# Kernel tuning notes

Measured on AMD Instinct MI355X. Metric: run time of the kernel, lower is better.

## Reference

```python
import jax, jax.numpy as jnp
import numpy as np

NHEAD = 16
HEAD_DIM = 64
EMBED_DIM = NHEAD * HEAD_DIM  # 1024
U, R, L, M = 2048, 256, 1024, 512


def setup_inputs() -> dict:
    key = jax.random.key(0)
    ks = jax.random.split(key, 11)
    D = EMBED_DIM
    inp = {
        "utterance": jax.random.normal(ks[0], (U, 1, D), jnp.float32),
        "right_context": jax.random.normal(ks[1], (R, 1, D), jnp.float32),
        "memory": jax.random.normal(ks[2], (M, 1, D), jnp.float32),
        "left_context_key": jax.random.normal(ks[3], (L, 1, D), jnp.float32),
        "left_context_val": jax.random.normal(ks[4], (L, 1, D), jnp.float32),
        "Wq": jax.random.normal(ks[5], (D, D), jnp.float32) * 0.02,
        "bq": jax.random.normal(ks[6], (D,), jnp.float32) * 0.02,
        "Wkv": jax.random.normal(ks[7], (2 * D, D), jnp.float32) * 0.02,
        "bkv": jax.random.normal(ks[8], (2 * D,), jnp.float32) * 0.02,
        "Wo": jax.random.normal(ks[9], (D, D), jnp.float32) * 0.02,
        "bo": jax.random.normal(ks[10], (D,), jnp.float32) * 0.02,
    }
    return inp


def reference(utterance, right_context, memory, left_context_key, left_context_val,
              Wq, bq, Wkv, bkv, Wo, bo):
    D = EMBED_DIM
    scaling = HEAD_DIM ** (-0.5)

    # query = Linear([right_context; utterance])  -> (Q, 1, D), Q = R + U
    q_in = jnp.concatenate([right_context, utterance], axis=0)
    query = q_in @ Wq.T + bq

    # key/value = Linear([memory; right_context; utterance]) split in two
    kv_in = jnp.concatenate([memory, right_context, utterance], axis=0)
    kv = kv_in @ Wkv.T + bkv  # (M+R+U, 1, 2D)
    k_new, v_new = kv[..., :D], kv[..., D:]

    # insert cached left-context key/value after [memory; right_context]
    key = jnp.concatenate([k_new[: M + R], left_context_key, k_new[M + R:]], axis=0)
    value = jnp.concatenate([v_new[: M + R], left_context_val, v_new[M + R:]], axis=0)

    Q = U + R
    KV = M + R + L + U
    # (T, 1, D) -> (nhead, T, head_dim)
    q = query.reshape(Q, NHEAD, HEAD_DIM).transpose(1, 0, 2)
    k = key.reshape(KV, NHEAD, HEAD_DIM).transpose(1, 0, 2)
    v = value.reshape(KV, NHEAD, HEAD_DIM).transpose(1, 0, 2)

    weights = jnp.einsum("hqd,hkd->hqk", q * scaling, k)  # (nhead, Q, KV)
    probs = jax.nn.softmax(weights, axis=-1)
    attn = jnp.einsum("hqk,hkd->hqd", probs, v)  # (nhead, Q, head_dim)

    attn = attn.transpose(1, 0, 2).reshape(Q, D)[:, None, :]  # (Q, 1, D)
    out = attn @ Wo.T + bo
    return out, key, value
```

## Files before the change

### kernel.cpp

```cpp
#include <hip/hip_runtime.h>
#include <hip/hip_bf16.h>

#define EMBED   1024
#define NHEADS  16
#define HDIM    64
#define U_LEN   2048
#define R_LEN   256
#define L_LEN   1024
#define M_LEN   512
#define Q_LEN   (U_LEN + R_LEN)
#define KV_LEN  (M_LEN + R_LEN + L_LEN + U_LEN)
#define X_ROWS  (M_LEN + R_LEN + U_LEN)
#define NPART   6
#define KV_PART (KV_LEN / NPART)

typedef __attribute__((ext_vector_type(8))) short short8;
typedef __attribute__((ext_vector_type(4))) float f32x4;
typedef __attribute__((ext_vector_type(16))) float f32x16;

#define QSCALE 0.180336880f

__device__ __forceinline__ void gl2lds16(const __hip_bfloat16* g, __hip_bfloat16* l) {
  __builtin_amdgcn_global_load_lds(
      (const __attribute__((address_space(1))) unsigned int*)g,
      (__attribute__((address_space(3))) unsigned int*)l, 16, 0, 0);
}

__device__ __forceinline__ unsigned pack_bf16(float a, float b) {
  unsigned r;
  asm("v_cvt_pk_bf16_f32 %0, %1, %2" : "=v"(r) : "v"(a), "v"(b));
  return r;
}

__device__ __forceinline__ void plane_swap(unsigned a, unsigned b, int h2,
                                           unsigned& lo, unsigned& hi) {
#if __has_builtin(__builtin_amdgcn_permlane32_swap)
  auto r = __builtin_amdgcn_permlane32_swap(a, b, false, false);
  lo = r[0]; hi = r[1];
#else
  unsigned s0 = h2 ? a : b;
  unsigned r0 = __shfl_xor(s0, 32, 64);
  lo = h2 ? r0 : a;
  hi = h2 ? b : r0;
#endif
}

__global__ __launch_bounds__(256) void prep_kernel(
    const float* __restrict__ mem, const float* __restrict__ rc,
    const float* __restrict__ utt, const float* __restrict__ lk,
    const float* __restrict__ lv, const float* __restrict__ Wq,
    const float* __restrict__ Wkv, const float* __restrict__ Wo,
    __hip_bfloat16* __restrict__ X, __hip_bfloat16* __restrict__ WB,
    __hip_bfloat16* __restrict__ WoB,
    float* __restrict__ key_out, float* __restrict__ val_out,
    __hip_bfloat16* __restrict__ k_bf, __hip_bfloat16* __restrict__ v_bf) {
  int b = blockIdx.x, tid = threadIdx.x;
  if (b < 2816) {
    int row = b, col = tid * 4;
    const float* src;
    if (row < M_LEN)              src = mem + row * EMBED;
    else if (row < M_LEN + R_LEN) src = rc + (row - M_LEN) * EMBED;
    else                          src = utt + (row - M_LEN - R_LEN) * EMBED;
    float4 v = *reinterpret_cast<const float4*>(src + col);
    __hip_bfloat16* d = X + (size_t)row * EMBED + col;
    d[0] = __float2bfloat16(v.x); d[1] = __float2bfloat16(v.y);
    d[2] = __float2bfloat16(v.z); d[3] = __float2bfloat16(v.w);
  } else if (b < 6912) {
    const float* src; __hip_bfloat16* dst;
    int blk;
    if (b < 3840)      { src = Wq;  dst = WB;                blk = b - 2816; }
    else if (b < 5888) { src = Wkv; dst = WB + 1024 * 1024;  blk = b - 3840; }
    else               { src = Wo;  dst = WoB;               blk = b - 5888; }
    int idx = blk * 1024 + tid * 4;
    float4 v = *reinterpret_cast<const float4*>(src + idx);
    dst[idx + 0] = __float2bfloat16(v.x);
    dst[idx + 1] = __float2bfloat16(v.y);
    dst[idx + 2] = __float2bfloat16(v.z);
    dst[idx + 3] = __float2bfloat16(v.w);
  } else {
    int row = b - 6912, c0 = tid * 4;
    int orow = 768 + row;
    float4 kv4 = *reinterpret_cast<const float4*>(lk + row * EMBED + c0);
    float4 vv4 = *reinterpret_cast<const float4*>(lv + row * EMBED + c0);
    *reinterpret_cast<float4*>(key_out + (size_t)orow * EMBED + c0) = kv4;
    *reinterpret_cast<float4*>(val_out + (size_t)orow * EMBED + c0) = vv4;
    __hip_bfloat16* kd = k_bf + (size_t)orow * EMBED + c0;
    __hip_bfloat16* vd = v_bf + (size_t)orow * EMBED + c0;
    kd[0] = __float2bfloat16(kv4.x); kd[1] = __float2bfloat16(kv4.y);
    kd[2] = __float2bfloat16(kv4.z); kd[3] = __float2bfloat16(kv4.w);
    vd[0] = __float2bfloat16(vv4.x); vd[1] = __float2bfloat16(vv4.y);
    vd[2] = __float2bfloat16(vv4.z); vd[3] = __float2bfloat16(vv4.w);
  }
}

__global__ __launch_bounds__(256) void transpose_kernel(
    const unsigned short* __restrict__ v_bf, unsigned short* __restrict__ vT) {
  __shared__ unsigned short T[64][72];
  int kt = blockIdx.x * 64, d0 = blockIdx.y * 64;
  int t = threadIdx.x;
  int r = t >> 3, c = (t & 7) * 8;
#pragma unroll
  for (int half = 0; half < 2; half++) {
    int kv = r + half * 32;
    short8 v = *reinterpret_cast<const short8*>(v_bf + (size_t)(kt + kv) * EMBED + d0 + c);
#pragma unroll
    for (int j = 0; j < 8; j++) T[c + j][kv] = (unsigned short)v[j];
  }
  __syncthreads();
#pragma unroll
  for (int half = 0; half < 2; half++) {
    int d = r + half * 32;
    *reinterpret_cast<short8*>(vT + (size_t)(d0 + d) * KV_LEN + kt + c) =
        *reinterpret_cast<const short8*>(&T[d][c]);
  }
}

__global__ __launch_bounds__(256) void gemm_qkv(
    const __hip_bfloat16* __restrict__ A, const __hip_bfloat16* __restrict__ B,
    const float* __restrict__ bq, const float* __restrict__ bkv,
    float* __restrict__ key_out, float* __restrict__ val_out,
    __hip_bfloat16* __restrict__ q_bf, __hip_bfloat16* __restrict__ k_bf,
    __hip_bfloat16* __restrict__ v_bf) {
  __shared__ __align__(16) __hip_bfloat16 As[128 * 64];
  __shared__ __align__(16) __hip_bfloat16 Bs[64 * 64];
  const int K = EMBED;
  int tid = threadIdx.x;
  int wave = tid >> 6, lane = tid & 63, quad = lane >> 4, l16 = lane & 15;
  int wm = wave >> 1, wn = wave & 1;
  int mbase = blockIdx.y * 128, nbase = blockIdx.x * 64;

  if (nbase < 1024 && mbase + 128 <= 512) return;

  int srow = tid >> 3;
  int scol = ((tid & 7) ^ (srow & 7)) * 8;
  const __hip_bfloat16* aG = A + (size_t)(mbase + srow) * K + scol;
  const __hip_bfloat16* bG = B + (size_t)(nbase + srow) * K + scol;
  int swz = l16 & 7;

  f32x4 acc[4][2] = {};
  for (int kt = 0; kt < K; kt += 64) {
    gl2lds16(aG + kt, As + tid * 8);
    gl2lds16(aG + (size_t)32 * K + kt, As + (tid + 256) * 8);
    gl2lds16(aG + (size_t)64 * K + kt, As + (tid + 512) * 8);
    gl2lds16(aG + (size_t)96 * K + kt, As + (tid + 768) * 8);
    gl2lds16(bG + kt, Bs + tid * 8);
    gl2lds16(bG + (size_t)32 * K + kt, Bs + (tid + 256) * 8);
    __syncthreads();
#pragma unroll
    for (int ks = 0; ks < 2; ks++) {
      short8 af[4], bfr[2];
#pragma unroll
      for (int i = 0; i < 4; i++)
        af[i] = *reinterpret_cast<const short8*>(
            As + (wm * 64 + i * 16 + l16) * 64 + ((ks * 4 + quad) ^ swz) * 8);
#pragma unroll
      for (int j = 0; j < 2; j++)
        bfr[j] = *reinterpret_cast<const short8*>(
            Bs + (wn * 32 + j * 16 + l16) * 64 + ((ks * 4 + quad) ^ swz) * 8);
#pragma unroll
      for (int i = 0; i < 4; i++)
#pragma unroll
        for (int j = 0; j < 2; j++)
          acc[i][j] = __builtin_amdgcn_mfma_f32_16x16x32_bf16(af[i], bfr[j], acc[i][j], 0, 0, 0);
    }
    __syncthreads();
  }

#pragma unroll
  for (int i = 0; i < 4; i++) {
    int rb = mbase + wm * 64 + i * 16 + quad * 4;
#pragma unroll
    for (int j = 0; j < 2; j++) {
      int cg = nbase + wn * 32 + j * 16 + l16;
      float bv = (cg < 1024) ? bq[cg] : bkv[cg - 1024];
#pragma unroll
      for (int reg = 0; reg < 4; reg++) {
        int rg = rb + reg;
        float val = acc[i][j][reg] + bv;
        if (cg < 1024) {
          if (rg >= 512)
            q_bf[(size_t)(rg - 512) * 1024 + cg] = __float2bfloat16(val * QSCALE);
        } else {
          int orow = (rg < 768) ? rg : rg + 1024;
          if (cg < 2048) {
            int cc = cg - 1024;
            key_out[(size_t)orow * 1024 + cc] = val;
            k_bf[(size_t)orow * 1024 + cc] = __float2bfloat16(val);
          } else {
            int cc = cg - 2048;
            val_out[(size_t)orow * 1024 + cc] = val;
            v_bf[(size_t)orow * 1024 + cc] = __float2bfloat16(val);
          }
        }
      }
    }
  }
}

__global__ __launch_bounds__(256) void gemm_out(
    const __hip_bfloat16* __restrict__ A, const __hip_bfloat16* __restrict__ B,
    float* __restrict__ partial) {
  __shared__ __align__(16) __hip_bfloat16 As[64 * 64];
  __shared__ __align__(16) __hip_bfloat16 Bs[64 * 64];
  const int K = EMBED, N = EMBED;
  int tid = threadIdx.x;
  int wave = tid >> 6, lane = tid & 63, quad = lane >> 4, l16 = lane & 15;
  int wm = wave >> 1, wn = wave & 1;
  int mbase = blockIdx.y * 64, nbase = blockIdx.x * 64;
  int kbase = blockIdx.z * 512;
  float* outp = partial + (size_t)blockIdx.z * Q_LEN * EMBED;

  int srow = tid >> 3;
  int scol = ((tid & 7) ^ (srow & 7)) * 8;
  const __hip_bfloat16* aG = A + (size_t)(mbase + srow) * K + kbase + scol;
  const __hip_bfloat16* bG = B + (size_t)(nbase + srow) * K + kbase + scol;
  int swz = l16 & 7;

  f32x4 acc[2][2] = {};
  for (int kt = 0; kt < 512; kt += 64) {
    gl2lds16(aG + kt, As + tid * 8);
    gl2lds16(aG + (size_t)32 * K + kt, As + (tid + 256) * 8);
    gl2lds16(bG + kt, Bs + tid * 8);
    gl2lds16(bG + (size_t)32 * K + kt, Bs + (tid + 256) * 8);
    __syncthreads();
#pragma unroll
    for (int ks = 0; ks < 2; ks++) {
      short8 af[2], bfr[2];
#pragma unroll
      for (int i = 0; i < 2; i++)
        af[i] = *reinterpret_cast<const short8*>(
            As + (wm * 32 + i * 16 + l16) * 64 + ((ks * 4 + quad) ^ swz) * 8);
#pragma unroll
      for (int j = 0; j < 2; j++)
        bfr[j] = *reinterpret_cast<const short8*>(
            Bs + (wn * 32 + j * 16 + l16) * 64 + ((ks * 4 + quad) ^ swz) * 8);
#pragma unroll
      for (int i = 0; i < 2; i++)
#pragma unroll
        for (int j = 0; j < 2; j++)
          acc[i][j] = __builtin_amdgcn_mfma_f32_16x16x32_bf16(af[i], bfr[j], acc[i][j], 0, 0, 0);
    }
    __syncthreads();
  }

#pragma unroll
  for (int i = 0; i < 2; i++) {
    int rb = mbase + wm * 32 + i * 16 + quad * 4;
#pragma unroll
    for (int j = 0; j < 2; j++) {
      int cg = nbase + wn * 32 + j * 16 + l16;
#pragma unroll
      for (int reg = 0; reg < 4; reg++)
        outp[(size_t)(rb + reg) * N + cg] = acc[i][j][reg];
    }
  }
}

__global__ __launch_bounds__(256) void reduce_out_kernel(
    const float* __restrict__ partial, const float* __restrict__ bias,
    float* __restrict__ outf) {
  int row = blockIdx.x, c = threadIdx.x * 4;
  float4 p0 = *reinterpret_cast<const float4*>(partial + (size_t)row * EMBED + c);
  float4 p1 = *reinterpret_cast<const float4*>(partial + (size_t)(Q_LEN + row) * EMBED + c);
  float4 bv = *reinterpret_cast<const float4*>(bias + c);
  float4 o;
  o.x = p0.x + p1.x + bv.x; o.y = p0.y + p1.y + bv.y;
  o.z = p0.z + p1.z + bv.z; o.w = p0.w + p1.w + bv.w;
  *reinterpret_cast<float4*>(outf + (size_t)row * EMBED + c) = o;
}

__global__ __launch_bounds__(256, 4) void attn_kernel(
    const __hip_bfloat16* __restrict__ q_bf, const __hip_bfloat16* __restrict__ k_bf,
    const __hip_bfloat16* __restrict__ vT,
    __hip_bfloat16* __restrict__ o_part, float* __restrict__ lsum) {
  __shared__ __align__(16) __hip_bfloat16 Ks[64][72];
  __shared__ __align__(16) __hip_bfloat16 VTs[64][72];
  int tid = threadIdx.x;
  int w = tid >> 6, lane = tid & 63, l31 = lane & 31, h2 = lane >> 5;

  int lid = blockIdx.x;
  int xcd = lid & 7, sfl = lid >> 3;
  int gi = sfl / 18, j = sfl - gi * 18;
  int g = gi * 8 + xcd;
  int part = g >> 4, h = g & 15;
  int qbase = j * 128;
  int qg = qbase + w * 32 + l31;

  short8 Qf[4];
#pragma unroll
  for (int ks = 0; ks < 4; ks++)
    Qf[ks] = *reinterpret_cast<const short8*>(
        q_bf + (size_t)qg * EMBED + h * HDIM + ks * 16 + h2 * 8);

  f32x16 ot[2] = {};
  float l_run = 0.f;

  int sr = tid >> 3, sc = (tid & 7) * 8;
  const int kv0 = part * KV_PART;

  short8 kr[2], vr[2];
#pragma unroll
  for (int half = 0; half < 2; half++) {
    int r = sr + half * 32;
    kr[half] = *reinterpret_cast<const short8*>(
        k_bf + (size_t)(kv0 + r) * EMBED + h * HDIM + sc);
    vr[half] = *reinterpret_cast<const short8*>(
        vT + (size_t)(h * HDIM + r) * KV_LEN + kv0 + sc);
  }

  for (int kt = kv0; kt < kv0 + KV_PART; kt += 64) {
    __syncthreads();
#pragma unroll
    for (int half = 0; half < 2; half++) {
      int r = sr + half * 32;
      *reinterpret_cast<short8*>(&Ks[r][sc]) = kr[half];
      *reinterpret_cast<short8*>(&VTs[r][sc]) = vr[half];
    }
    __syncthreads();
    if (kt + 64 < kv0 + KV_PART) {
#pragma unroll
      for (int half = 0; half < 2; half++) {
        int r = sr + half * 32;
        kr[half] = *reinterpret_cast<const short8*>(
            k_bf + (size_t)(kt + 64 + r) * EMBED + h * HDIM + sc);
        vr[half] = *reinterpret_cast<const short8*>(
            vT + (size_t)(h * HDIM + r) * KV_LEN + kt + 64 + sc);
      }
    }

#pragma unroll
    for (int kvs = 0; kvs < 2; kvs++) {
      f32x16 s = {};
      __builtin_amdgcn_s_setprio(1);
#pragma unroll
      for (int ks = 0; ks < 4; ks++) {
        short8 ak = *reinterpret_cast<const short8*>(&Ks[kvs * 32 + l31][ks * 16 + h2 * 8]);
        s = __builtin_amdgcn_mfma_f32_32x32x16_bf16(ak, Qf[ks], s, 0, 0, 0);
      }
      __builtin_amdgcn_s_setprio(0);
      unsigned u[4][2];
#pragma unroll
      for (int gq = 0; gq < 4; gq++) {
        float p0 = __builtin_amdgcn_exp2f(s[4 * gq + 0]);
        float p1 = __builtin_amdgcn_exp2f(s[4 * gq + 1]);
        float p2 = __builtin_amdgcn_exp2f(s[4 * gq + 2]);
        float p3 = __builtin_amdgcn_exp2f(s[4 * gq + 3]);
        l_run += (p0 + p1) + (p2 + p3);
        u[gq][0] = pack_bf16(p0, p1);
        u[gq][1] = pack_bf16(p2, p3);
      }
#pragma unroll
      for (int half = 0; half < 2; half++) {
        int c = kvs * 2 + half;
        int gA = 2 * half, gB = 2 * half + 1;
        uint4 fr;
        plane_swap(u[gA][0], u[gB][0], h2, fr.x, fr.z);
        plane_swap(u[gA][1], u[gB][1], h2, fr.y, fr.w);
        short8 pf = __builtin_bit_cast(short8, fr);
        __builtin_amdgcn_s_setprio(1);
#pragma unroll
        for (int ds = 0; ds < 2; ds++) {
          short8 av = *reinterpret_cast<const short8*>(&VTs[ds * 32 + l31][c * 16 + h2 * 8]);
          ot[ds] = __builtin_amdgcn_mfma_f32_32x32x16_bf16(av, pf, ot[ds], 0, 0, 0);
        }
        __builtin_amdgcn_s_setprio(0);
      }
    }
  }

  l_run += __shfl_xor(l_run, 32, 64);
  float inv = 1.0f / l_run;

  size_t orow = (size_t)part * Q_LEN + qg;
#pragma unroll
  for (int ds = 0; ds < 2; ds++)
#pragma unroll
    for (int gq = 0; gq < 4; gq++) {
      uint2 pk;
      pk.x = pack_bf16(ot[ds][4 * gq + 0] * inv, ot[ds][4 * gq + 1] * inv);
      pk.y = pack_bf16(ot[ds][4 * gq + 2] * inv, ot[ds][4 * gq + 3] * inv);
      *reinterpret_cast<uint2*>(
          o_part + orow * 1024 + h * HDIM + ds * 32 + gq * 8 + h2 * 4) = pk;
    }
  if (lane < 32)
    lsum[orow * NHEADS + h] = l_run;
}

__global__ __launch_bounds__(256) void merge_kernel(
    const __hip_bfloat16* __restrict__ o_part, const float* __restrict__ lsum,
    __hip_bfloat16* __restrict__ attn_bf) {
  int q = blockIdx.x;
  int c = threadIdx.x * 4;
  int h = c >> 6;
  float wt[NPART], L = 0.f;
#pragma unroll
  for (int p = 0; p < NPART; p++) {
    wt[p] = lsum[((size_t)p * Q_LEN + q) * NHEADS + h];
    L += wt[p];
  }
  float invL = 1.0f / L;
  float acc[4] = {0.f, 0.f, 0.f, 0.f};
#pragma unroll
  for (int p = 0; p < NPART; p++) {
    __hip_bfloat16 v[4];
    *reinterpret_cast<uint2*>(v) =
        *reinterpret_cast<const uint2*>(o_part + ((size_t)p * Q_LEN + q) * 1024 + c);
#pragma unroll
    for (int jj = 0; jj < 4; jj++) acc[jj] += wt[p] * __bfloat162float(v[jj]);
  }
  uint2 pk;
  pk.x = pack_bf16(acc[0] * invL, acc[1] * invL);
  pk.y = pack_bf16(acc[2] * invL, acc[3] * invL);
  *reinterpret_cast<uint2*>(attn_bf + (size_t)q * 1024 + c) = pk;
}


extern "C" void kernel_launch(void* const* d_in, const int* in_sizes, int n_in,
                              void* d_out, int out_size, void* d_ws, size_t ws_size,
                              hipStream_t stream) {
  const float* utt = (const float*)d_in[0];
  const float* rc  = (const float*)d_in[1];
  const float* mem = (const float*)d_in[2];
  const float* lk  = (const float*)d_in[3];
  const float* lv  = (const float*)d_in[4];
  const float* Wq  = (const float*)d_in[5];
  const float* bq  = (const float*)d_in[6];
  const float* Wkv = (const float*)d_in[7];
  const float* bkv = (const float*)d_in[8];
  const float* Wo  = (const float*)d_in[9];
  const float* bo  = (const float*)d_in[10];

  float* out_f   = (float*)d_out;
  float* key_out = out_f + Q_LEN * EMBED;
  float* val_out = key_out + KV_LEN * EMBED;

  char* ws = (char*)d_ws;
  size_t off = 0;
  __hip_bfloat16* X_bf   = (__hip_bfloat16*)(ws + off); off += (size_t)X_ROWS * EMBED * 2;
  __hip_bfloat16* WB_bf  = (__hip_bfloat16*)(ws + off); off += (size_t)3 * EMBED * EMBED * 2;
  __hip_bfloat16* Wo_bf  = (__hip_bfloat16*)(ws + off); off += (size_t)EMBED * EMBED * 2;
  __hip_bfloat16* q_bf   = (__hip_bfloat16*)(ws + off); off += (size_t)Q_LEN * EMBED * 2;
  __hip_bfloat16* k_bf   = (__hip_bfloat16*)(ws + off); off += (size_t)KV_LEN * EMBED * 2;
  __hip_bfloat16* vT_bf  = (__hip_bfloat16*)(ws + off); off += (size_t)EMBED * KV_LEN * 2;
  __hip_bfloat16* o_part = (__hip_bfloat16*)(ws + off); off += (size_t)NPART * Q_LEN * EMBED * 2;
  __hip_bfloat16* attn_bf = X_bf;
  float* lsum = (float*)WB_bf;
  __hip_bfloat16* v_bf = o_part;
  float* out_partial = (float*)q_bf;
  (void)off; (void)ws_size; (void)in_sizes; (void)n_in; (void)out_size;

  prep_kernel<<<7936, 256, 0, stream>>>(mem, rc, utt, lk, lv, Wq, Wkv, Wo,
                                        X_bf, WB_bf, Wo_bf,
                                        key_out, val_out, k_bf, v_bf);
  gemm_qkv<<<dim3(3 * EMBED / 64, X_ROWS / 128), 256, 0, stream>>>(
      X_bf, WB_bf, bq, bkv, key_out, val_out, q_bf, k_bf, v_bf);
  transpose_kernel<<<dim3(KV_LEN / 64, EMBED / 64), 256, 0, stream>>>(
      (const unsigned short*)v_bf, (unsigned short*)vT_bf);
  attn_kernel<<<dim3((Q_LEN / 128) * NHEADS * NPART), 256, 0, stream>>>(
      q_bf, k_bf, vT_bf, o_part, lsum);
  merge_kernel<<<Q_LEN, 256, 0, stream>>>(o_part, lsum, attn_bf);
  gemm_out<<<dim3(EMBED / 64, Q_LEN / 64, 2), 256, 0, stream>>>(
      attn_bf, Wo_bf, out_partial);
  reduce_out_kernel<<<Q_LEN, 256, 0, stream>>>(out_partial, bo, out_f);
}
```

Before: 212.3 us.

## Enlarge QKV GEMM tiles, drop split-K in out-proj, pack bf16 stores, swizzle grids

The QKV projection GEMM moves from 128x64 to 128x128 tiles, so each wave computes a 4x4 MFMA block and reuses more of its LDS data. Both GEMMs now use a 1D grid remapped so consecutive blocks land on the same XCD. The output projection no longer splits K in two: it runs the full K loop, adds the bias itself, and the separate reduce kernel is removed. The prep kernel writes packed bf16 pairs as 8-byte stores instead of scalar 2-byte stores. The risks are fewer blocks in flight (528 and 576) with more registers per thread, and longer per-block K loops in the output GEMM.

```diff
diff --git a/kernel.cpp b/kernel.cpp
--- a/kernel.cpp
+++ b/kernel.cpp
@@ -62,9 +62,8 @@
     else if (row < M_LEN + R_LEN) src = rc + (row - M_LEN) * EMBED;
     else                          src = utt + (row - M_LEN - R_LEN) * EMBED;
     float4 v = *reinterpret_cast<const float4*>(src + col);
-    __hip_bfloat16* d = X + (size_t)row * EMBED + col;
-    d[0] = __float2bfloat16(v.x); d[1] = __float2bfloat16(v.y);
-    d[2] = __float2bfloat16(v.z); d[3] = __float2bfloat16(v.w);
+    uint2 pk; pk.x = pack_bf16(v.x, v.y); pk.y = pack_bf16(v.z, v.w);
+    *reinterpret_cast<uint2*>(X + (size_t)row * EMBED + col) = pk;
   } else if (b < 6912) {
     const float* src; __hip_bfloat16* dst;
     int blk;
@@ -73,10 +72,8 @@
     else               { src = Wo;  dst = WoB;               blk = b - 5888; }
     int idx = blk * 1024 + tid * 4;
     float4 v = *reinterpret_cast<const float4*>(src + idx);
-    dst[idx + 0] = __float2bfloat16(v.x);
-    dst[idx + 1] = __float2bfloat16(v.y);
-    dst[idx + 2] = __float2bfloat16(v.z);
-    dst[idx + 3] = __float2bfloat16(v.w);
+    uint2 pk; pk.x = pack_bf16(v.x, v.y); pk.y = pack_bf16(v.z, v.w);
+    *reinterpret_cast<uint2*>(dst + idx) = pk;
   } else {
     int row = b - 6912, c0 = tid * 4;
     int orow = 768 + row;
@@ -84,12 +81,11 @@
     float4 vv4 = *reinterpret_cast<const float4*>(lv + row * EMBED + c0);
     *reinterpret_cast<float4*>(key_out + (size_t)orow * EMBED + c0) = kv4;
     *reinterpret_cast<float4*>(val_out + (size_t)orow * EMBED + c0) = vv4;
-    __hip_bfloat16* kd = k_bf + (size_t)orow * EMBED + c0;
-    __hip_bfloat16* vd = v_bf + (size_t)orow * EMBED + c0;
-    kd[0] = __float2bfloat16(kv4.x); kd[1] = __float2bfloat16(kv4.y);
-    kd[2] = __float2bfloat16(kv4.z); kd[3] = __float2bfloat16(kv4.w);
-    vd[0] = __float2bfloat16(vv4.x); vd[1] = __float2bfloat16(vv4.y);
-    vd[2] = __float2bfloat16(vv4.z); vd[3] = __float2bfloat16(vv4.w);
+    uint2 pk, pv;
+    pk.x = pack_bf16(kv4.x, kv4.y); pk.y = pack_bf16(kv4.z, kv4.w);
+    pv.x = pack_bf16(vv4.x, vv4.y); pv.y = pack_bf16(vv4.z, vv4.w);
+    *reinterpret_cast<uint2*>(k_bf + (size_t)orow * EMBED + c0) = pk;
+    *reinterpret_cast<uint2*>(v_bf + (size_t)orow * EMBED + c0) = pv;
   }
 }
 
@@ -122,14 +118,18 @@
     __hip_bfloat16* __restrict__ q_bf, __hip_bfloat16* __restrict__ k_bf,
     __hip_bfloat16* __restrict__ v_bf) {
   __shared__ __align__(16) __hip_bfloat16 As[128 * 64];
-  __shared__ __align__(16) __hip_bfloat16 Bs[64 * 64];
+  __shared__ __align__(16) __hip_bfloat16 Bs[128 * 64];
   const int K = EMBED;
   int tid = threadIdx.x;
   int wave = tid >> 6, lane = tid & 63, quad = lane >> 4, l16 = lane & 15;
   int wm = wave >> 1, wn = wave & 1;
-  int mbase = blockIdx.y * 128, nbase = blockIdx.x * 64;
-
-  if (nbase < 1024 && mbase + 128 <= 512) return;
+
+  int lid = blockIdx.x;
+  int gsw = (lid & 7) * 66 + (lid >> 3);
+  int bx = gsw / 22, by = gsw % 22;
+  int mbase = by * 128, nbase = bx * 128;
+
+  if (nbase + 128 <= 1024 && mbase + 128 <= 512) return;
 
   int srow = tid >> 3;
   int scol = ((tid & 7) ^ (srow & 7)) * 8;
@@ -137,30 +137,29 @@
   const __hip_bfloat16* bG = B + (size_t)(nbase + srow) * K + scol;
   int swz = l16 & 7;
 
-  f32x4 acc[4][2] = {};
+  f32x4 acc[4][4] = {};
   for (int kt = 0; kt < K; kt += 64) {
-    gl2lds16(aG + kt, As + tid * 8);
-    gl2lds16(aG + (size_t)32 * K + kt, As + (tid + 256) * 8);
-    gl2lds16(aG + (size_t)64 * K + kt, As + (tid + 512) * 8);
-    gl2lds16(aG + (size_t)96 * K + kt, As + (tid + 768) * 8);
-    gl2lds16(bG + kt, Bs + tid * 8);
-    gl2lds16(bG + (size_t)32 * K + kt, Bs + (tid + 256) * 8);
+#pragma unroll
+    for (int i = 0; i < 4; i++) {
+      gl2lds16(aG + (size_t)(32 * i) * K + kt, As + (tid + 256 * i) * 8);
+      gl2lds16(bG + (size_t)(32 * i) * K + kt, Bs + (tid + 256 * i) * 8);
+    }
     __syncthreads();
 #pragma unroll
     for (int ks = 0; ks < 2; ks++) {
-      short8 af[4], bfr[2];
+      short8 af[4], bfr[4];
 #pragma unroll
       for (int i = 0; i < 4; i++)
         af[i] = *reinterpret_cast<const short8*>(
             As + (wm * 64 + i * 16 + l16) * 64 + ((ks * 4 + quad) ^ swz) * 8);
 #pragma unroll
-      for (int j = 0; j < 2; j++)
+      for (int j = 0; j < 4; j++)
         bfr[j] = *reinterpret_cast<const short8*>(
-            Bs + (wn * 32 + j * 16 + l16) * 64 + ((ks * 4 + quad) ^ swz) * 8);
+            Bs + (wn * 64 + j * 16 + l16) * 64 + ((ks * 4 + quad) ^ swz) * 8);
 #pragma unroll
       for (int i = 0; i < 4; i++)
 #pragma unroll
-        for (int j = 0; j < 2; j++)
+        for (int j = 0; j < 4; j++)
           acc[i][j] = __builtin_amdgcn_mfma_f32_16x16x32_bf16(af[i], bfr[j], acc[i][j], 0, 0, 0);
     }
     __syncthreads();
@@ -170,8 +169,8 @@
   for (int i = 0; i < 4; i++) {
     int rb = mbase + wm * 64 + i * 16 + quad * 4;
 #pragma unroll
-    for (int j = 0; j < 2; j++) {
-      int cg = nbase + wn * 32 + j * 16 + l16;
+    for (int j = 0; j < 4; j++) {
+      int cg = nbase + wn * 64 + j * 16 + l16;
       float bv = (cg < 1024) ? bq[cg] : bkv[cg - 1024];
 #pragma unroll
       for (int reg = 0; reg < 4; reg++) {
@@ -199,25 +198,27 @@
 
 __global__ __launch_bounds__(256) void gemm_out(
     const __hip_bfloat16* __restrict__ A, const __hip_bfloat16* __restrict__ B,
-    float* __restrict__ partial) {
+    const float* __restrict__ bias, float* __restrict__ outf) {
   __shared__ __align__(16) __hip_bfloat16 As[64 * 64];
   __shared__ __align__(16) __hip_bfloat16 Bs[64 * 64];
   const int K = EMBED, N = EMBED;
   int tid = threadIdx.x;
   int wave = tid >> 6, lane = tid & 63, quad = lane >> 4, l16 = lane & 15;
   int wm = wave >> 1, wn = wave & 1;
-  int mbase = blockIdx.y * 64, nbase = blockIdx.x * 64;
-  int kbase = blockIdx.z * 512;
-  float* outp = partial + (size_t)blockIdx.z * Q_LEN * EMBED;
+
+  int lid = blockIdx.x;
+  int gsw = (lid & 7) * 72 + (lid >> 3);
+  int bx = gsw / 36, by = gsw % 36;
+  int mbase = by * 64, nbase = bx * 64;
 
   int srow = tid >> 3;
   int scol = ((tid & 7) ^ (srow & 7)) * 8;
-  const __hip_bfloat16* aG = A + (size_t)(mbase + srow) * K + kbase + scol;
-  const __hip_bfloat16* bG = B + (size_t)(nbase + srow) * K + kbase + scol;
+  const __hip_bfloat16* aG = A + (size_t)(mbase + srow) * K + scol;
+  const __hip_bfloat16* bG = B + (size_t)(nbase + srow) * K + scol;
   int swz = l16 & 7;
 
   f32x4 acc[2][2] = {};
-  for (int kt = 0; kt < 512; kt += 64) {
+  for (int kt = 0; kt < K; kt += 64) {
     gl2lds16(aG + kt, As + tid * 8);
     gl2lds16(aG + (size_t)32 * K + kt, As + (tid + 256) * 8);
     gl2lds16(bG + kt, Bs + tid * 8);
@@ -249,24 +250,12 @@
 #pragma unroll
     for (int j = 0; j < 2; j++) {
       int cg = nbase + wn * 32 + j * 16 + l16;
+      float bv = bias[cg];
 #pragma unroll
       for (int reg = 0; reg < 4; reg++)
-        outp[(size_t)(rb + reg) * N + cg] = acc[i][j][reg];
-    }
-  }
-}
-
-__global__ __launch_bounds__(256) void reduce_out_kernel(
-    const float* __restrict__ partial, const float* __restrict__ bias,
-    float* __restrict__ outf) {
-  int row = blockIdx.x, c = threadIdx.x * 4;
-  float4 p0 = *reinterpret_cast<const float4*>(partial + (size_t)row * EMBED + c);
-  float4 p1 = *reinterpret_cast<const float4*>(partial + (size_t)(Q_LEN + row) * EMBED + c);
-  float4 bv = *reinterpret_cast<const float4*>(bias + c);
-  float4 o;
-  o.x = p0.x + p1.x + bv.x; o.y = p0.y + p1.y + bv.y;
-  o.z = p0.z + p1.z + bv.z; o.w = p0.w + p1.w + bv.w;
-  *reinterpret_cast<float4*>(outf + (size_t)row * EMBED + c) = o;
+        outf[(size_t)(rb + reg) * N + cg] = acc[i][j][reg] + bv;
+    }
+  }
 }
 
 __global__ __launch_bounds__(256, 4) void attn_kernel(
@@ -446,20 +435,17 @@
   __hip_bfloat16* attn_bf = X_bf;
   float* lsum = (float*)WB_bf;
   __hip_bfloat16* v_bf = o_part;
-  float* out_partial = (float*)q_bf;
   (void)off; (void)ws_size; (void)in_sizes; (void)n_in; (void)out_size;
 
   prep_kernel<<<7936, 256, 0, stream>>>(mem, rc, utt, lk, lv, Wq, Wkv, Wo,
                                         X_bf, WB_bf, Wo_bf,
                                         key_out, val_out, k_bf, v_bf);
-  gemm_qkv<<<dim3(3 * EMBED / 64, X_ROWS / 128), 256, 0, stream>>>(
+  gemm_qkv<<<528, 256, 0, stream>>>(
       X_bf, WB_bf, bq, bkv, key_out, val_out, q_bf, k_bf, v_bf);
   transpose_kernel<<<dim3(KV_LEN / 64, EMBED / 64), 256, 0, stream>>>(
       (const unsigned short*)v_bf, (unsigned short*)vT_bf);
   attn_kernel<<<dim3((Q_LEN / 128) * NHEADS * NPART), 256, 0, stream>>>(
       q_bf, k_bf, vT_bf, o_part, lsum);
   merge_kernel<<<Q_LEN, 256, 0, stream>>>(o_part, lsum, attn_bf);
-  gemm_out<<<dim3(EMBED / 64, Q_LEN / 64, 2), 256, 0, stream>>>(
-      attn_bf, Wo_bf, out_partial);
-  reduce_out_kernel<<<Q_LEN, 256, 0, stream>>>(out_partial, bo, out_f);
-}
+  gemm_out<<<576, 256, 0, stream>>>(attn_bf, Wo_bf, bo, out_f);
+}
```

Result: slower. 220.0 us (+3.6%).
